# Performance work log

Hardware: AMD Instinct MI355X
Metric: run time of the kernel (lower is better)

Reference implementation:

```python
import jax, jax.numpy as jnp
import numpy as np

DIM = 64        # feature channels of x
HEADS = 4
POS_DIM = 3
NUM_IDS = 8
STR_IN = 512    # strength_linear input size
B, S, W = 4, 1024, 8   # batch, sequence (S1), source-views (S2)


def setup_inputs() -> dict:
    key = jax.random.key(0)
    ks = jax.random.split(key, 18)
    stdv = 1.0 / np.sqrt(DIM * DIM)  # embedding init per module
    d8 = DIM // 8
    u = lambda k, shp, s: jax.random.uniform(k, shp, jnp.float32, -s, s)
    return {
        "x": jax.random.normal(ks[0], (B, DIM, S, W), jnp.float32),
        "pos": jax.random.normal(ks[1], (B, S, POS_DIM), jnp.float32),
        "strength": jax.random.normal(ks[2], (STR_IN,), jnp.float32),
        "embed_id1": 3,
        "q_emb_w": u(ks[3], (NUM_IDS, DIM * DIM), stdv),
        "k_emb_w": u(ks[4], (NUM_IDS, DIM * DIM), stdv),
        "v_emb_w": u(ks[5], (NUM_IDS, DIM * DIM), stdv),
        "pos_w1": u(ks[6], (POS_DIM, POS_DIM), 1.0 / np.sqrt(POS_DIM)),
        "pos_b1": u(ks[7], (POS_DIM,), 1.0 / np.sqrt(POS_DIM)),
        "pos_w2": u(ks[8], (d8, POS_DIM), 1.0 / np.sqrt(POS_DIM)),
        "pos_b2": u(ks[9], (d8,), 1.0 / np.sqrt(POS_DIM)),
        "head_w": u(ks[10], (HEADS, d8), 1.0 / np.sqrt(d8)),
        "head_b": u(ks[11], (HEADS,), 1.0 / np.sqrt(d8)),
        "gate": jnp.ones((HEADS,), jnp.float32),
        "out_w": u(ks[12], (DIM, DIM), 1.0 / np.sqrt(DIM)),
        "out_b": u(ks[13], (DIM,), 1.0 / np.sqrt(DIM)),
        "str_w": u(ks[14], (DIM, STR_IN), 1.0 / np.sqrt(STR_IN)),
        "str_b": u(ks[15], (DIM,), 1.0 / np.sqrt(STR_IN)),
    }


def reference(x, pos, strength, embed_id1, q_emb_w, k_emb_w, v_emb_w,
              pos_w1, pos_b1, pos_w2, pos_b2, head_w, head_b, gate,
              out_w, out_b, str_w, str_b):
    # strength projection: Linear(512, dim)
    s = strength @ str_w.T + str_b                    # [dim]
    xt = jnp.transpose(x, (0, 2, 3, 1))               # [B, S, W, dim]
    qe = q_emb_w[embed_id1].reshape(DIM, DIM)
    ke = k_emb_w[embed_id1].reshape(DIM, DIM)
    ve = v_emb_w[embed_id1].reshape(DIM, DIM)

    def proj(emb):
        y = xt @ emb.T + s                            # [B, S, W, dim]
        # collapse (W, dim) -> (heads, head_dim), heads to axis 1
        y = y.reshape(B, S, HEADS, -1)
        return jnp.transpose(y, (0, 2, 1, 3))         # [B, H, S, hd]

    q, k, v = proj(qe), proj(ke), proj(ve)
    hd = q.shape[-1]
    attn = jax.nn.softmax(jnp.einsum("bhsd,bhtd->bhst", q, k) / np.sqrt(hd), axis=-1)

    # relative-position attention branch
    ph = jax.nn.relu(pos @ pos_w1.T + pos_b1) @ pos_w2.T + pos_b2   # [B, S, dim//8]
    diff = ph[:, :, None, :] - ph[:, None, :, :]                    # [B, S, S, dim//8]
    pos_attn = jnp.transpose(diff @ head_w.T + head_b, (0, 3, 1, 2))
    pos_attn = jax.nn.softmax(pos_attn, axis=-1)                    # [B, H, S, S]

    g = jax.nn.sigmoid(gate).reshape(1, -1, 1, 1)
    attn = (1.0 - g) * attn + g * pos_attn
    attn = attn / jnp.sum(attn, axis=-1, keepdims=True)

    out = jnp.einsum("bhst,bhtd->bhsd", attn, v)      # [B, H, S, hd]
    out = jnp.transpose(out, (0, 2, 1, 3)).reshape(B, S, W, DIM)
    return out @ out_w.T + out_b                      # [B, S, W, dim]
```

## Files before the change

kernel.cpp:

```cpp
#include <hip/hip_runtime.h>
#include <math.h>
#include <stdint.h>

#define B_ 4
#define S_ 1024
#define F_ 512
#define HD 128
#define SOFT_C 4.0f

typedef __attribute__((ext_vector_type(8))) short short8;
typedef __attribute__((ext_vector_type(4))) float f32x4;
typedef __attribute__((ext_vector_type(4))) unsigned int u32x4;
typedef __attribute__((ext_vector_type(2))) unsigned int u32x2;

__device__ __forceinline__ unsigned short f2bf(float f) {
    unsigned int u = __float_as_uint(f);
    u = (u + 0x7FFFu + ((u >> 16) & 1u)) >> 16;
    return (unsigned short)u;
}
__device__ __forceinline__ float bf2f(unsigned int s) {
    return __uint_as_float(s << 16);
}
__device__ __forceinline__ void pack_hilo(const float* v, u32x4& hi, u32x4& lo) {
    #pragma unroll
    for (int p = 0; p < 4; ++p) {
        unsigned int h0 = f2bf(v[2 * p]), h1 = f2bf(v[2 * p + 1]);
        float l0 = v[2 * p] - bf2f(h0), l1 = v[2 * p + 1] - bf2f(h1);
        hi[p] = h0 | (h1 << 16);
        lo[p] = (unsigned int)f2bf(l0) | ((unsigned int)f2bf(l1) << 16);
    }
}

__global__ __launch_bounds__(256) void k_prep(
    const int* __restrict__ embed_id,
    const float* __restrict__ qw, const float* __restrict__ kw,
    const float* __restrict__ vw, const float* __restrict__ ow,
    const float* __restrict__ pos,
    const float* __restrict__ pw1, const float* __restrict__ pb1,
    const float* __restrict__ pw2, const float* __restrict__ pb2,
    const float* __restrict__ head_w,
    const float* __restrict__ strength, const float* __restrict__ str_w,
    const float* __restrict__ str_b,
    unsigned short* __restrict__ packs,
    float* __restrict__ sv, float* __restrict__ svq,
    float* __restrict__ p_g)
{
    __shared__ float red_s[4][4];
    __shared__ float inv_s[4];
    const int blk = blockIdx.x, tid = threadIdx.x;
    const float SCALE = 0.08838834764831845f;

    if (blk < 4) {
        const int id = embed_id[0];
        const float* src = (blk == 0 ? qw + id * 4096 : blk == 1 ? kw + id * 4096
                            : blk == 2 ? vw + id * 4096 : ow);
        const float scale = (blk == 0) ? SCALE : 1.0f;
        unsigned short* hi = packs + blk * 8192;
        unsigned short* lo = hi + 4096;
        for (int i = tid; i < 4096; i += 256) {
            float v = src[i] * scale;
            unsigned short h = f2bf(v);
            hi[i] = h;
            lo[i] = f2bf(v - bf2f(h));
        }
    } else if (blk < 8) {
        const int b = blk - 4;
        const int wv = tid >> 6;
        float w1_[9], b1_[3], w2_[24], b2_[8], hw_[32];
        #pragma unroll
        for (int i = 0; i < 9; ++i)  w1_[i] = pw1[i];
        #pragma unroll
        for (int i = 0; i < 3; ++i)  b1_[i] = pb1[i];
        #pragma unroll
        for (int i = 0; i < 24; ++i) w2_[i] = pw2[i];
        #pragma unroll
        for (int i = 0; i < 8; ++i)  b2_[i] = pb2[i];
        #pragma unroll
        for (int i = 0; i < 32; ++i) hw_[i] = head_w[i];

        float ev[4][4];
        float ps[4] = {0.f, 0.f, 0.f, 0.f};
        #pragma unroll
        for (int k = 0; k < 4; ++k) {
            const int t = k * 256 + tid;
            float p0 = pos[(b * S_ + t) * 3 + 0];
            float p1 = pos[(b * S_ + t) * 3 + 1];
            float p2 = pos[(b * S_ + t) * 3 + 2];
            float h0 = fmaxf(0.f, p0 * w1_[0] + p1 * w1_[1] + p2 * w1_[2] + b1_[0]);
            float h1 = fmaxf(0.f, p0 * w1_[3] + p1 * w1_[4] + p2 * w1_[5] + b1_[1]);
            float h2 = fmaxf(0.f, p0 * w1_[6] + p1 * w1_[7] + p2 * w1_[8] + b1_[2]);
            float ph[8];
            #pragma unroll
            for (int o8 = 0; o8 < 8; ++o8)
                ph[o8] = h0 * w2_[o8 * 3] + h1 * w2_[o8 * 3 + 1] + h2 * w2_[o8 * 3 + 2] + b2_[o8];
            #pragma unroll
            for (int h = 0; h < 4; ++h) {
                float A = 0.f;
                #pragma unroll
                for (int o8 = 0; o8 < 8; ++o8) A += ph[o8] * hw_[h * 8 + o8];
                ev[k][h] = __expf(-A - 1.0f);
                ps[h] += ev[k][h];
            }
        }
        #pragma unroll
        for (int h = 0; h < 4; ++h)
            #pragma unroll
            for (int off = 1; off < 64; off <<= 1)
                ps[h] += __shfl_xor(ps[h], off);
        if ((tid & 63) == 0)
            #pragma unroll
            for (int h = 0; h < 4; ++h) red_s[wv][h] = ps[h];
        __syncthreads();
        if (tid < 4)
            inv_s[tid] = 1.f / (red_s[0][tid] + red_s[1][tid] + red_s[2][tid] + red_s[3][tid]);
        __syncthreads();
        #pragma unroll
        for (int k = 0; k < 4; ++k)
            #pragma unroll
            for (int h = 0; h < 4; ++h)
                p_g[(b * 4 + h) * S_ + k * 256 + tid] = ev[k][h] * inv_s[h];
    } else {
        __shared__ float part_s[4][64];
        const int c = tid & 63, pr = tid >> 6;
        const float* wrow = str_w + c * 512 + pr * 128;
        const float* st   = strength + pr * 128;
        float acc = 0.f;
        #pragma unroll
        for (int j4 = 0; j4 < 32; ++j4) {
            f32x4 wv4 = *(const f32x4*)(wrow + j4 * 4);
            f32x4 s4  = *(const f32x4*)(st + j4 * 4);
            acc += wv4[0] * s4[0] + wv4[1] * s4[1] + wv4[2] * s4[2] + wv4[3] * s4[3];
        }
        part_s[pr][c] = acc;
        __syncthreads();
        if (tid < 64) {
            float v = part_s[0][tid] + part_s[1][tid] + part_s[2][tid]
                    + part_s[3][tid] + str_b[tid];
            sv[tid] = v;
            svq[tid] = v * SCALE;
        }
    }
}

__global__ __launch_bounds__(256) void k_qkv(
    const float* __restrict__ x,
    const unsigned short* __restrict__ packs,
    const float* __restrict__ sv, const float* __restrict__ svq,
    const float* __restrict__ p_g,
    unsigned short* __restrict__ yqh, unsigned short* __restrict__ ykh,
    unsigned short* __restrict__ yvt2, float* __restrict__ xbar)
{
    __shared__ float xr_s[4][8];
    const int tid  = threadIdx.x;
    const int wv   = tid >> 6;
    const int lane = tid & 63;
    const int quad = lane >> 4;
    const int l15  = lane & 15;

    if (blockIdx.x >= 512) {
        const int bi = blockIdx.x - 512;
        const int b = bi >> 6, c = bi & 63;
        const float* xc = x + (size_t)b * 524288 + c * 8192;
        const float* pb = p_g + b * 4096;
        float acc[8] = {};
        #pragma unroll
        for (int rr = 0; rr < 4; ++rr) {
            const int s = tid * 4 + rr;
            f32x4 x0 = *(const f32x4*)(xc + s * 8);
            f32x4 x1 = *(const f32x4*)(xc + s * 8 + 4);
            float p0 = pb[s], p1 = pb[1024 + s], p2 = pb[2048 + s], p3 = pb[3072 + s];
            acc[0] += p0 * x0[0]; acc[1] += p0 * x0[1];
            acc[2] += p1 * x0[2]; acc[3] += p1 * x0[3];
            acc[4] += p2 * x1[0]; acc[5] += p2 * x1[1];
            acc[6] += p3 * x1[2]; acc[7] += p3 * x1[3];
        }
        #pragma unroll
        for (int j = 0; j < 8; ++j)
            #pragma unroll
            for (int off = 1; off < 64; off <<= 1)
                acc[j] += __shfl_xor(acc[j], off);
        if (lane == 0)
            #pragma unroll
            for (int j = 0; j < 8; ++j) xr_s[wv][j] = acc[j];
        __syncthreads();
        if (tid < 8)
            xbar[(b * 8 + tid) * 64 + c] = xr_s[0][tid] + xr_s[1][tid]
                                         + xr_s[2][tid] + xr_s[3][tid];
        return;
    }

    const int r0   = blockIdx.x * 64 + wv * 16;
    const int b    = r0 >> 13;
    const int rloc = (r0 & 8191) + l15;
    const float* xb = x + (size_t)b * 524288;

    u32x4 xhi[2], xlo[2];
    #pragma unroll
    for (int kc = 0; kc < 2; ++kc) {
        float xv[8];
        #pragma unroll
        for (int j = 0; j < 8; ++j)
            xv[j] = xb[(kc * 32 + quad * 8 + j) * 8192 + rloc];
        pack_hilo(xv, xhi[kc], xlo[kc]);
    }

    float svq_l[4], sv_l[4];
    #pragma unroll
    for (int nt = 0; nt < 4; ++nt) {
        svq_l[nt] = svq[nt * 16 + l15];
        sv_l[nt]  = sv[nt * 16 + l15];
    }
    f32x4 svA[4];
    #pragma unroll
    for (int mt = 0; mt < 4; ++mt)
        svA[mt] = *(const f32x4*)(sv + mt * 16 + quad * 4);

    int idxq[4];
    #pragma unroll
    for (int rr = 0; rr < 4; ++rr) {
        const int rl = quad * 4 + rr;
        const int w_ = rl & 7;
        const int s_loc = ((r0 & 8191) >> 3) + (rl >> 3);
        idxq[rr] = (b * 4 + (w_ >> 1)) * 131072 + s_loc * 128 + (w_ & 1) * 64 + l15;
    }
    const int row_g = r0 + l15;
    const int s_idx = (row_g >> 3) & 1023;
    const int w_idx = row_g & 7;
    const int bh    = b * 4 + (w_idx >> 1);
    const int dbase = (w_idx & 1) * 64;
    unsigned short* vtb = yvt2 + (size_t)bh * 131072 + (s_idx >> 6) * 8192
                        + (size_t)dbase * 64 + (s_idx & 63);

    #pragma unroll
    for (int mat = 0; mat < 2; ++mat) {
        const unsigned short* mh = packs + mat * 8192;
        const unsigned short* ml = mh + 4096;
        f32x4 acc[4] = {};
        #pragma unroll
        for (int kc = 0; kc < 2; ++kc)
            #pragma unroll
            for (int nt = 0; nt < 4; ++nt) {
                const int off = (nt * 16 + l15) * 64 + kc * 32 + quad * 8;
                u32x4 ehi = *(const u32x4*)(mh + off);
                u32x4 elo = *(const u32x4*)(ml + off);
                acc[nt] = __builtin_amdgcn_mfma_f32_16x16x32_bf16(
                    __builtin_bit_cast(short8, xhi[kc]),
                    __builtin_bit_cast(short8, ehi), acc[nt], 0, 0, 0);
                acc[nt] = __builtin_amdgcn_mfma_f32_16x16x32_bf16(
                    __builtin_bit_cast(short8, xlo[kc]),
                    __builtin_bit_cast(short8, ehi), acc[nt], 0, 0, 0);
                acc[nt] = __builtin_amdgcn_mfma_f32_16x16x32_bf16(
                    __builtin_bit_cast(short8, xhi[kc]),
                    __builtin_bit_cast(short8, elo), acc[nt], 0, 0, 0);
            }
        unsigned short* y = (mat == 0 ? yqh : ykh);
        const float* svp = (mat == 0 ? svq_l : sv_l);
        #pragma unroll
        for (int nt = 0; nt < 4; ++nt)
            #pragma unroll
            for (int rr = 0; rr < 4; ++rr)
                y[(size_t)idxq[rr] + nt * 16] = f2bf(acc[nt][rr] + svp[nt]);
    }
    {
        const unsigned short* mh = packs + 2 * 8192;
        const unsigned short* ml = mh + 4096;
        f32x4 acc[4] = {};
        #pragma unroll
        for (int kc = 0; kc < 2; ++kc)
            #pragma unroll
            for (int mt = 0; mt < 4; ++mt) {
                const int off = (mt * 16 + l15) * 64 + kc * 32 + quad * 8;
                u32x4 ehi = *(const u32x4*)(mh + off);
                u32x4 elo = *(const u32x4*)(ml + off);
                acc[mt] = __builtin_amdgcn_mfma_f32_16x16x32_bf16(
                    __builtin_bit_cast(short8, ehi),
                    __builtin_bit_cast(short8, xhi[kc]), acc[mt], 0, 0, 0);
                acc[mt] = __builtin_amdgcn_mfma_f32_16x16x32_bf16(
                    __builtin_bit_cast(short8, ehi),
                    __builtin_bit_cast(short8, xlo[kc]), acc[mt], 0, 0, 0);
                acc[mt] = __builtin_amdgcn_mfma_f32_16x16x32_bf16(
                    __builtin_bit_cast(short8, elo),
                    __builtin_bit_cast(short8, xhi[kc]), acc[mt], 0, 0, 0);
            }
        #pragma unroll
        for (int mt = 0; mt < 4; ++mt)
            #pragma unroll
            for (int rr = 0; rr < 4; ++rr) {
                const int c = mt * 16 + quad * 4 + rr;
                vtb[(size_t)c * 64] = f2bf(acc[mt][rr] + svA[mt][rr]);
            }
    }
}

__global__ __launch_bounds__(256, 4) void k_attn(
    const unsigned short* __restrict__ yqh, const unsigned short* __restrict__ ykh,
    const unsigned short* __restrict__ yvt2,
    const float* __restrict__ xbar, const float* __restrict__ vw,
    const int* __restrict__ embed_id, const float* __restrict__ sv_g,
    const float* __restrict__ gate,
    const unsigned short* __restrict__ packs,
    const float* __restrict__ ow, const float* __restrict__ ob,
    float* __restrict__ out)
{
    __shared__ __align__(16) unsigned short kx[64 * 136];
    __shared__ __align__(16) unsigned short vx[128 * 72];
    __shared__ float vbar_s[128];
    __shared__ float vproj_s[128];
    __shared__ float lsh[2][16];

    const int tid  = threadIdx.x;
    const int w    = tid >> 6;
    const int lane = tid & 63;
    const int quad = lane >> 4;
    const int l15  = lane & 15;
    const int bh = blockIdx.x & 15, qt = blockIdx.x >> 4;
    const int b = bh >> 2, h = bh & 3;
    const int s0 = qt * 16;
    const int th = w >> 1;
    const int dh = w & 1;

    const unsigned short* ykb = ykh + (size_t)bh * 131072;
    const unsigned short* yvb = yvt2 + (size_t)bh * 131072;
    const float gf = 1.f / (1.f + __expf(-gate[h]));

    if (tid < 128) {
        const int c = tid & 63, wloc = tid >> 6;
        const float* ver = vw + embed_id[0] * 4096 + c * 64;
        const float* xbr = xbar + (b * 8 + h * 2 + wloc) * 64;
        float a = sv_g[c];
        #pragma unroll
        for (int j4 = 0; j4 < 16; ++j4) {
            f32x4 e4 = *(const f32x4*)(ver + j4 * 4);
            f32x4 x4 = *(const f32x4*)(xbr + j4 * 4);
            a += e4[0] * x4[0] + e4[1] * x4[1] + e4[2] * x4[2] + e4[3] * x4[3];
        }
        vbar_s[wloc * 64 + c] = a;
    }

    u32x4 qf[4];
    #pragma unroll
    for (int kc = 0; kc < 4; ++kc)
        qf[kc] = *(const u32x4*)(yqh + (size_t)bh * 131072
                 + (s0 + l15) * 128 + kc * 32 + quad * 8);

    u32x4 kst[4], vst[4];
    #pragma unroll
    for (int r = 0; r < 4; ++r) {
        kst[r] = *(const u32x4*)(ykb + r * 2048 + tid * 8);
        vst[r] = *(const u32x4*)(yvb + r * 2048 + tid * 8);
    }

    __syncthreads();
    if (tid < 128) {
        const int cp = tid & 63, w2 = tid >> 6;
        const float* owr = ow + cp * 64;
        const float* vb = vbar_s + w2 * 64;
        float a = 0.f;
        #pragma unroll
        for (int j4 = 0; j4 < 16; ++j4) {
            f32x4 o4 = *(const f32x4*)(owr + j4 * 4);
            f32x4 v4 = *(const f32x4*)(vb + j4 * 4);
            a += o4[0] * v4[0] + o4[1] * v4[1] + o4[2] * v4[2] + o4[3] * v4[3];
        }
        vproj_s[tid] = gf * a + ob[cp];
    }

    f32x4 o[4] = {};
    float lsum = 0.f;
    const int srcA = ((quad & 1) << 5) + l15;
    const int t0loc = th * 32;

    for (int it = 0; it < 16; ++it) {
        #pragma unroll
        for (int r = 0; r < 4; ++r) {
            const int off = r * 2048 + tid * 8;
            *(u32x4*)&kx[(off >> 7) * 136 + (off & 127)] = kst[r];
            *(u32x4*)&vx[(off >> 6) * 72 + (off & 63)] = vst[r];
        }
        __syncthreads();
        if (it < 15) {
            const unsigned short* ksrc = ykb + (it + 1) * 8192;
            const unsigned short* vsrc = yvb + (it + 1) * 8192;
            #pragma unroll
            for (int r = 0; r < 4; ++r)
                kst[r] = *(const u32x4*)(ksrc + r * 2048 + tid * 8);
            #pragma unroll
            for (int r = 0; r < 4; ++r)
                vst[r] = *(const u32x4*)(vsrc + r * 2048 + tid * 8);
        }

        f32x4 sa0 = {}, sa1 = {};
        #pragma unroll
        for (int kc = 0; kc < 4; ++kc) {
            u32x4 a0 = *(const u32x4*)&kx[(t0loc + l15) * 136 + kc * 32 + quad * 8];
            sa0 = __builtin_amdgcn_mfma_f32_16x16x32_bf16(
                __builtin_bit_cast(short8, a0),
                __builtin_bit_cast(short8, qf[kc]), sa0, 0, 0, 0);
        }
        #pragma unroll
        for (int kc = 0; kc < 4; ++kc) {
            u32x4 a1 = *(const u32x4*)&kx[(t0loc + 16 + l15) * 136 + kc * 32 + quad * 8];
            sa1 = __builtin_amdgcn_mfma_f32_16x16x32_bf16(
                __builtin_bit_cast(short8, a1),
                __builtin_bit_cast(short8, qf[kc]), sa1, 0, 0, 0);
        }

        float p0[4], p1[4];
        #pragma unroll
        for (int r = 0; r < 4; ++r) {
            p0[r] = __expf(sa0[r] - SOFT_C);
            p1[r] = __expf(sa1[r] - SOFT_C);
            lsum += p0[r] + p1[r];
        }

        unsigned int pk00 = (unsigned int)f2bf(p0[0]) | ((unsigned int)f2bf(p0[1]) << 16);
        unsigned int pk01 = (unsigned int)f2bf(p0[2]) | ((unsigned int)f2bf(p0[3]) << 16);
        unsigned int pk10 = (unsigned int)f2bf(p1[0]) | ((unsigned int)f2bf(p1[1]) << 16);
        unsigned int pk11 = (unsigned int)f2bf(p1[2]) | ((unsigned int)f2bf(p1[3]) << 16);
        unsigned int sel0 = (quad < 2) ? pk00 : pk10;
        unsigned int sel1 = (quad < 2) ? pk01 : pk11;
        u32x4 pf;
        pf[0] = (unsigned int)__shfl((int)sel0, srcA);
        pf[1] = (unsigned int)__shfl((int)sel1, srcA);
        pf[2] = (unsigned int)__shfl((int)sel0, srcA + 16);
        pf[3] = (unsigned int)__shfl((int)sel1, srcA + 16);

        #pragma unroll
        for (int dt = 0; dt < 4; ++dt) {
            u32x4 vf = *(const u32x4*)&vx[(dh * 64 + dt * 16 + l15) * 72
                                           + t0loc + quad * 8];
            o[dt] = __builtin_amdgcn_mfma_f32_16x16x32_bf16(
                __builtin_bit_cast(short8, vf),
                __builtin_bit_cast(short8, pf), o[dt], 0, 0, 0);
        }
        __syncthreads();
    }

    lsum += __shfl_xor(lsum, 16);
    lsum += __shfl_xor(lsum, 32);
    float* cmb = (float*)kx;
    if (th == 1) {
        #pragma unroll
        for (int dt = 0; dt < 4; ++dt)
            *(f32x4*)&cmb[(dh * 16 + l15) * 68 + dt * 16 + quad * 4] = o[dt];
        if (quad == 0) lsh[dh][l15] = lsum;
    }
    __syncthreads();
    if (th == 0) {
        #pragma unroll
        for (int dt = 0; dt < 4; ++dt) {
            f32x4 p = *(const f32x4*)&cmb[(dh * 16 + l15) * 68 + dt * 16 + quad * 4];
            o[dt] += p;
        }
        lsum += lsh[dh][l15];
        const float cf = (1.f - gf) / lsum;

        unsigned short* yst = (unsigned short*)vx + dh * 4352;
        #pragma unroll
        for (int dt = 0; dt < 4; ++dt) {
            unsigned int hh[4];
            unsigned short ll[4];
            #pragma unroll
            for (int r = 0; r < 4; ++r) {
                float y = cf * o[dt][r];
                hh[r] = f2bf(y);
                ll[r] = f2bf(y - bf2f(hh[r]));
            }
            const int dloc = dt * 16 + quad * 4;
            u32x2 ph_, pl_;
            ph_[0] = hh[0] | (hh[1] << 16);
            ph_[1] = hh[2] | (hh[3] << 16);
            pl_[0] = (unsigned int)ll[0] | ((unsigned int)ll[1] << 16);
            pl_[1] = (unsigned int)ll[2] | ((unsigned int)ll[3] << 16);
            *(u32x2*)&yst[l15 * 68 + dloc] = ph_;
            *(u32x2*)&yst[1088 + l15 * 68 + dloc] = pl_;
        }
        u32x4 ybh[2], ybl[2];
        #pragma unroll
        for (int kc = 0; kc < 2; ++kc) {
            ybh[kc] = *(const u32x4*)&yst[l15 * 68 + kc * 32 + quad * 8];
            ybl[kc] = *(const u32x4*)&yst[1088 + l15 * 68 + kc * 32 + quad * 8];
        }
        const unsigned short* owh = packs + 3 * 8192;
        const unsigned short* owl = owh + 4096;
        f32x4 accp[4] = {};
        #pragma unroll
        for (int kc = 0; kc < 2; ++kc)
            #pragma unroll
            for (int mt = 0; mt < 4; ++mt) {
                const int off = (mt * 16 + l15) * 64 + kc * 32 + quad * 8;
                u32x4 ahi = *(const u32x4*)(owh + off);
                u32x4 alo = *(const u32x4*)(owl + off);
                accp[mt] = __builtin_amdgcn_mfma_f32_16x16x32_bf16(
                    __builtin_bit_cast(short8, ahi),
                    __builtin_bit_cast(short8, ybh[kc]), accp[mt], 0, 0, 0);
                accp[mt] = __builtin_amdgcn_mfma_f32_16x16x32_bf16(
                    __builtin_bit_cast(short8, ahi),
                    __builtin_bit_cast(short8, ybl[kc]), accp[mt], 0, 0, 0);
                accp[mt] = __builtin_amdgcn_mfma_f32_16x16x32_bf16(
                    __builtin_bit_cast(short8, alo),
                    __builtin_bit_cast(short8, ybh[kc]), accp[mt], 0, 0, 0);
            }
        const int sQ = s0 + l15;
        float* op = out + ((size_t)((b * S_ + sQ) * 8 + 2 * h + dh)) * 64;
        #pragma unroll
        for (int mt = 0; mt < 4; ++mt) {
            f32x4 vp = *(const f32x4*)&vproj_s[dh * 64 + mt * 16 + quad * 4];
            f32x4 rv = accp[mt] + vp;
            *(f32x4*)(op + mt * 16 + quad * 4) = rv;
        }
    }
}

extern "C" void kernel_launch(void* const* d_in, const int* in_sizes, int n_in,
                              void* d_out, int out_size, void* d_ws, size_t ws_size,
                              hipStream_t stream) {
    (void)in_sizes; (void)n_in; (void)out_size; (void)ws_size;
    const float* x        = (const float*)d_in[0];
    const float* pos      = (const float*)d_in[1];
    const float* strength = (const float*)d_in[2];
    const int*   embed_id = (const int*)d_in[3];
    const float* qw       = (const float*)d_in[4];
    const float* kw       = (const float*)d_in[5];
    const float* vw       = (const float*)d_in[6];
    const float* pw1      = (const float*)d_in[7];
    const float* pb1      = (const float*)d_in[8];
    const float* pw2      = (const float*)d_in[9];
    const float* pb2      = (const float*)d_in[10];
    const float* head_w   = (const float*)d_in[11];
    const float* gate     = (const float*)d_in[13];
    const float* out_w    = (const float*)d_in[14];
    const float* out_b    = (const float*)d_in[15];
    const float* str_w    = (const float*)d_in[16];
    const float* str_b    = (const float*)d_in[17];
    float* out = (float*)d_out;

    unsigned short* yqh   = (unsigned short*)d_ws;
    unsigned short* ykh   = yqh + 2097152;
    unsigned short* yvt2  = ykh + 2097152;
    unsigned short* packs = yvt2 + 2097152;
    float* sv   = (float*)(packs + 8 * 4096);
    float* svq  = sv + 64;
    float* p_g  = svq + 64;
    float* xbar = p_g + 16384;

    k_prep<<<9, 256, 0, stream>>>(embed_id, qw, kw, vw, out_w, pos,
                                  pw1, pb1, pw2, pb2, head_w,
                                  strength, str_w, str_b, packs, sv, svq, p_g);
    k_qkv<<<768, 256, 0, stream>>>(x, packs, sv, svq, p_g, yqh, ykh, yvt2, xbar);
    k_attn<<<1024, 256, 0, stream>>>(yqh, ykh, yvt2, xbar, vw, embed_id, sv,
                                     gate, packs, out_w, out_b, out);
}
```

Baseline: 165.5 us.

## Store K/V in MFMA fragment order and stream them from global without LDS

The QKV kernel now writes K and V directly in the per-lane MFMA fragment layout, so the attention kernel can load operands straight from global memory into registers with a one-step register prefetch instead of staging tiles through LDS with barriers. Each attention block now handles 32 queries (each wave owns a 16-query x 64-dim slice over all keys), so the cross-wave partial-sum combine and the grid halves to 512 blocks. This removes LDS traffic and per-iteration syncthreads, but each wave now reads K/V from global/L2 on its own, raising cache traffic and register pressure. The occupancy hint in launch bounds is also dropped.

```diff
diff --git a/kernel.cpp b/kernel.cpp
--- a/kernel.cpp
+++ b/kernel.cpp
@@ -147,8 +147,8 @@
     const unsigned short* __restrict__ packs,
     const float* __restrict__ sv, const float* __restrict__ svq,
     const float* __restrict__ p_g,
-    unsigned short* __restrict__ yqh, unsigned short* __restrict__ ykh,
-    unsigned short* __restrict__ yvt2, float* __restrict__ xbar)
+    unsigned short* __restrict__ yqh, unsigned short* __restrict__ kfrag,
+    unsigned short* __restrict__ vfrag, float* __restrict__ xbar)
 {
     __shared__ float xr_s[4][8];
     const int tid  = threadIdx.x;
@@ -216,20 +216,25 @@
         svA[mt] = *(const f32x4*)(sv + mt * 16 + quad * 4);
 
     int idxq[4];
+    size_t idxk[4];
     #pragma unroll
     for (int rr = 0; rr < 4; ++rr) {
         const int rl = quad * 4 + rr;
-        const int w_ = rl & 7;
-        const int s_loc = ((r0 & 8191) >> 3) + (rl >> 3);
-        idxq[rr] = (b * 4 + (w_ >> 1)) * 131072 + s_loc * 128 + (w_ & 1) * 64 + l15;
+        const int row_g2 = r0 + rl;
+        const int s = (row_g2 & 8191) >> 3;
+        const int w_ = row_g2 & 7;
+        const int bh = ((row_g2 >> 13) * 4) + (w_ >> 1);
+        idxq[rr] = (bh * 131072) + s * 128 + (w_ & 1) * 64 + l15;
+        idxk[rr] = (size_t)(bh * 64 + (s >> 4)) * 2048 + (s & 15) * 8
+                 + (w_ & 1) * 1024 + (l15 >> 3) * 128 + (l15 & 7);
     }
     const int row_g = r0 + l15;
     const int s_idx = (row_g >> 3) & 1023;
     const int w_idx = row_g & 7;
-    const int bh    = b * 4 + (w_idx >> 1);
+    const int bhv   = (row_g >> 13) * 4 + (w_idx >> 1);
     const int dbase = (w_idx & 1) * 64;
-    unsigned short* vtb = yvt2 + (size_t)bh * 131072 + (s_idx >> 6) * 8192
-                        + (size_t)dbase * 64 + (s_idx & 63);
+    const size_t vbase = (size_t)(bhv * 32 + (s_idx >> 5)) * 4096
+                       + ((s_idx >> 3) & 3) * 8 + (s_idx & 7);
 
     #pragma unroll
     for (int mat = 0; mat < 2; ++mat) {
@@ -253,13 +258,19 @@
                     __builtin_bit_cast(short8, xhi[kc]),
                     __builtin_bit_cast(short8, elo), acc[nt], 0, 0, 0);
             }
-        unsigned short* y = (mat == 0 ? yqh : ykh);
-        const float* svp = (mat == 0 ? svq_l : sv_l);
-        #pragma unroll
-        for (int nt = 0; nt < 4; ++nt)
-            #pragma unroll
-            for (int rr = 0; rr < 4; ++rr)
-                y[(size_t)idxq[rr] + nt * 16] = f2bf(acc[nt][rr] + svp[nt]);
+        if (mat == 0) {
+            #pragma unroll
+            for (int nt = 0; nt < 4; ++nt)
+                #pragma unroll
+                for (int rr = 0; rr < 4; ++rr)
+                    yqh[(size_t)idxq[rr] + nt * 16] = f2bf(acc[nt][rr] + svq_l[nt]);
+        } else {
+            #pragma unroll
+            for (int nt = 0; nt < 4; ++nt)
+                #pragma unroll
+                for (int rr = 0; rr < 4; ++rr)
+                    kfrag[idxk[rr] + nt * 256] = f2bf(acc[nt][rr] + sv_l[nt]);
+        }
     }
     {
         const unsigned short* mh = packs + 2 * 8192;
@@ -286,15 +297,16 @@
         for (int mt = 0; mt < 4; ++mt)
             #pragma unroll
             for (int rr = 0; rr < 4; ++rr) {
-                const int c = mt * 16 + quad * 4 + rr;
-                vtb[(size_t)c * 64] = f2bf(acc[mt][rr] + svA[mt][rr]);
+                const int dd = dbase + mt * 16 + quad * 4 + rr;
+                vfrag[vbase + (dd >> 4) * 512 + (dd & 15) * 32] =
+                    f2bf(acc[mt][rr] + svA[mt][rr]);
             }
     }
 }
 
-__global__ __launch_bounds__(256, 4) void k_attn(
-    const unsigned short* __restrict__ yqh, const unsigned short* __restrict__ ykh,
-    const unsigned short* __restrict__ yvt2,
+__global__ __launch_bounds__(256) void k_attn(
+    const unsigned short* __restrict__ yqh, const unsigned short* __restrict__ kfrag,
+    const unsigned short* __restrict__ vfrag,
     const float* __restrict__ xbar, const float* __restrict__ vw,
     const int* __restrict__ embed_id, const float* __restrict__ sv_g,
     const float* __restrict__ gate,
@@ -302,11 +314,9 @@
     const float* __restrict__ ow, const float* __restrict__ ob,
     float* __restrict__ out)
 {
-    __shared__ __align__(16) unsigned short kx[64 * 136];
-    __shared__ __align__(16) unsigned short vx[128 * 72];
+    __shared__ __align__(16) unsigned short yst_s[4 * 4352];
     __shared__ float vbar_s[128];
     __shared__ float vproj_s[128];
-    __shared__ float lsh[2][16];
 
     const int tid  = threadIdx.x;
     const int w    = tid >> 6;
@@ -315,12 +325,12 @@
     const int l15  = lane & 15;
     const int bh = blockIdx.x & 15, qt = blockIdx.x >> 4;
     const int b = bh >> 2, h = bh & 3;
-    const int s0 = qt * 16;
-    const int th = w >> 1;
+    const int s0 = qt * 32;
+    const int qh = w >> 1;
     const int dh = w & 1;
 
-    const unsigned short* ykb = ykh + (size_t)bh * 131072;
-    const unsigned short* yvb = yvt2 + (size_t)bh * 131072;
+    const unsigned short* kb = kfrag + (size_t)bh * 131072;
+    const unsigned short* vb = vfrag + (size_t)bh * 131072;
     const float gf = 1.f / (1.f + __expf(-gate[h]));
 
     if (tid < 128) {
@@ -336,74 +346,72 @@
         }
         vbar_s[wloc * 64 + c] = a;
     }
-
-    u32x4 qf[4];
-    #pragma unroll
-    for (int kc = 0; kc < 4; ++kc)
-        qf[kc] = *(const u32x4*)(yqh + (size_t)bh * 131072
-                 + (s0 + l15) * 128 + kc * 32 + quad * 8);
-
-    u32x4 kst[4], vst[4];
-    #pragma unroll
-    for (int r = 0; r < 4; ++r) {
-        kst[r] = *(const u32x4*)(ykb + r * 2048 + tid * 8);
-        vst[r] = *(const u32x4*)(yvb + r * 2048 + tid * 8);
-    }
-
     __syncthreads();
     if (tid < 128) {
         const int cp = tid & 63, w2 = tid >> 6;
         const float* owr = ow + cp * 64;
-        const float* vb = vbar_s + w2 * 64;
+        const float* vbp = vbar_s + w2 * 64;
         float a = 0.f;
         #pragma unroll
         for (int j4 = 0; j4 < 16; ++j4) {
             f32x4 o4 = *(const f32x4*)(owr + j4 * 4);
-            f32x4 v4 = *(const f32x4*)(vb + j4 * 4);
+            f32x4 v4 = *(const f32x4*)(vbp + j4 * 4);
             a += o4[0] * v4[0] + o4[1] * v4[1] + o4[2] * v4[2] + o4[3] * v4[3];
         }
         vproj_s[tid] = gf * a + ob[cp];
     }
+    __syncthreads();
+
+    u32x4 qf[4];
+    #pragma unroll
+    for (int kc = 0; kc < 4; ++kc)
+        qf[kc] = *(const u32x4*)(yqh + (size_t)bh * 131072
+                 + (s0 + qh * 16 + l15) * 128 + kc * 32 + quad * 8);
+
+    const int kl = quad * 128 + l15 * 8;
+    const int vl = l15 * 32 + quad * 8;
 
     f32x4 o[4] = {};
     float lsum = 0.f;
     const int srcA = ((quad & 1) << 5) + l15;
-    const int t0loc = th * 32;
-
-    for (int it = 0; it < 16; ++it) {
-        #pragma unroll
-        for (int r = 0; r < 4; ++r) {
-            const int off = r * 2048 + tid * 8;
-            *(u32x4*)&kx[(off >> 7) * 136 + (off & 127)] = kst[r];
-            *(u32x4*)&vx[(off >> 6) * 72 + (off & 63)] = vst[r];
-        }
-        __syncthreads();
-        if (it < 15) {
-            const unsigned short* ksrc = ykb + (it + 1) * 8192;
-            const unsigned short* vsrc = yvb + (it + 1) * 8192;
-            #pragma unroll
-            for (int r = 0; r < 4; ++r)
-                kst[r] = *(const u32x4*)(ksrc + r * 2048 + tid * 8);
-            #pragma unroll
-            for (int r = 0; r < 4; ++r)
-                vst[r] = *(const u32x4*)(vsrc + r * 2048 + tid * 8);
+
+    u32x4 k0c[4], k1c[4], vvc[4];
+    #pragma unroll
+    for (int kc = 0; kc < 4; ++kc) {
+        k0c[kc] = *(const u32x4*)(kb + kc * 512 + kl);
+        k1c[kc] = *(const u32x4*)(kb + 2048 + kc * 512 + kl);
+    }
+    #pragma unroll
+    for (int dt = 0; dt < 4; ++dt)
+        vvc[dt] = *(const u32x4*)(vb + (dh * 4 + dt) * 512 + vl);
+
+    #pragma unroll 2
+    for (int it = 0; it < 32; ++it) {
+        u32x4 k0n[4], k1n[4], vvn[4];
+        if (it < 31) {
+            const unsigned short* kbn = kb + (size_t)(it + 1) * 4096;
+            const unsigned short* vbn = vb + (size_t)(it + 1) * 4096;
+            #pragma unroll
+            for (int kc = 0; kc < 4; ++kc) {
+                k0n[kc] = *(const u32x4*)(kbn + kc * 512 + kl);
+                k1n[kc] = *(const u32x4*)(kbn + 2048 + kc * 512 + kl);
+            }
+            #pragma unroll
+            for (int dt = 0; dt < 4; ++dt)
+                vvn[dt] = *(const u32x4*)(vbn + (dh * 4 + dt) * 512 + vl);
         }
 
         f32x4 sa0 = {}, sa1 = {};
         #pragma unroll
-        for (int kc = 0; kc < 4; ++kc) {
-            u32x4 a0 = *(const u32x4*)&kx[(t0loc + l15) * 136 + kc * 32 + quad * 8];
+        for (int kc = 0; kc < 4; ++kc)
             sa0 = __builtin_amdgcn_mfma_f32_16x16x32_bf16(
-                __builtin_bit_cast(short8, a0),
+                __builtin_bit_cast(short8, k0c[kc]),
                 __builtin_bit_cast(short8, qf[kc]), sa0, 0, 0, 0);
-        }
-        #pragma unroll
-        for (int kc = 0; kc < 4; ++kc) {
-            u32x4 a1 = *(const u32x4*)&kx[(t0loc + 16 + l15) * 136 + kc * 32 + quad * 8];
+        #pragma unroll
+        for (int kc = 0; kc < 4; ++kc)
             sa1 = __builtin_amdgcn_mfma_f32_16x16x32_bf16(
-                __builtin_bit_cast(short8, a1),
+                __builtin_bit_cast(short8, k1c[kc]),
                 __builtin_bit_cast(short8, qf[kc]), sa1, 0, 0, 0);
-        }
 
         float p0[4], p1[4];
         #pragma unroll
@@ -426,89 +434,74 @@
         pf[3] = (unsigned int)__shfl((int)sel1, srcA + 16);
 
         #pragma unroll
-        for (int dt = 0; dt < 4; ++dt) {
-            u32x4 vf = *(const u32x4*)&vx[(dh * 64 + dt * 16 + l15) * 72
-                                           + t0loc + quad * 8];
+        for (int dt = 0; dt < 4; ++dt)
             o[dt] = __builtin_amdgcn_mfma_f32_16x16x32_bf16(
-                __builtin_bit_cast(short8, vf),
+                __builtin_bit_cast(short8, vvc[dt]),
                 __builtin_bit_cast(short8, pf), o[dt], 0, 0, 0);
-        }
-        __syncthreads();
+
+        #pragma unroll
+        for (int kc = 0; kc < 4; ++kc) { k0c[kc] = k0n[kc]; k1c[kc] = k1n[kc]; }
+        #pragma unroll
+        for (int dt = 0; dt < 4; ++dt) vvc[dt] = vvn[dt];
     }
 
     lsum += __shfl_xor(lsum, 16);
     lsum += __shfl_xor(lsum, 32);
-    float* cmb = (float*)kx;
-    if (th == 1) {
-        #pragma unroll
-        for (int dt = 0; dt < 4; ++dt)
-            *(f32x4*)&cmb[(dh * 16 + l15) * 68 + dt * 16 + quad * 4] = o[dt];
-        if (quad == 0) lsh[dh][l15] = lsum;
-    }
-    __syncthreads();
-    if (th == 0) {
-        #pragma unroll
-        for (int dt = 0; dt < 4; ++dt) {
-            f32x4 p = *(const f32x4*)&cmb[(dh * 16 + l15) * 68 + dt * 16 + quad * 4];
-            o[dt] += p;
-        }
-        lsum += lsh[dh][l15];
-        const float cf = (1.f - gf) / lsum;
-
-        unsigned short* yst = (unsigned short*)vx + dh * 4352;
-        #pragma unroll
-        for (int dt = 0; dt < 4; ++dt) {
-            unsigned int hh[4];
-            unsigned short ll[4];
-            #pragma unroll
-            for (int r = 0; r < 4; ++r) {
-                float y = cf * o[dt][r];
-                hh[r] = f2bf(y);
-                ll[r] = f2bf(y - bf2f(hh[r]));
-            }
-            const int dloc = dt * 16 + quad * 4;
-            u32x2 ph_, pl_;
-            ph_[0] = hh[0] | (hh[1] << 16);
-            ph_[1] = hh[2] | (hh[3] << 16);
-            pl_[0] = (unsigned int)ll[0] | ((unsigned int)ll[1] << 16);
-            pl_[1] = (unsigned int)ll[2] | ((unsigned int)ll[3] << 16);
-            *(u32x2*)&yst[l15 * 68 + dloc] = ph_;
-            *(u32x2*)&yst[1088 + l15 * 68 + dloc] = pl_;
-        }
-        u32x4 ybh[2], ybl[2];
-        #pragma unroll
-        for (int kc = 0; kc < 2; ++kc) {
-            ybh[kc] = *(const u32x4*)&yst[l15 * 68 + kc * 32 + quad * 8];
-            ybl[kc] = *(const u32x4*)&yst[1088 + l15 * 68 + kc * 32 + quad * 8];
-        }
-        const unsigned short* owh = packs + 3 * 8192;
-        const unsigned short* owl = owh + 4096;
-        f32x4 accp[4] = {};
-        #pragma unroll
-        for (int kc = 0; kc < 2; ++kc)
-            #pragma unroll
-            for (int mt = 0; mt < 4; ++mt) {
-                const int off = (mt * 16 + l15) * 64 + kc * 32 + quad * 8;
-                u32x4 ahi = *(const u32x4*)(owh + off);
-                u32x4 alo = *(const u32x4*)(owl + off);
-                accp[mt] = __builtin_amdgcn_mfma_f32_16x16x32_bf16(
-                    __builtin_bit_cast(short8, ahi),
-                    __builtin_bit_cast(short8, ybh[kc]), accp[mt], 0, 0, 0);
-                accp[mt] = __builtin_amdgcn_mfma_f32_16x16x32_bf16(
-                    __builtin_bit_cast(short8, ahi),
-                    __builtin_bit_cast(short8, ybl[kc]), accp[mt], 0, 0, 0);
-                accp[mt] = __builtin_amdgcn_mfma_f32_16x16x32_bf16(
-                    __builtin_bit_cast(short8, alo),
-                    __builtin_bit_cast(short8, ybh[kc]), accp[mt], 0, 0, 0);
-            }
-        const int sQ = s0 + l15;
-        float* op = out + ((size_t)((b * S_ + sQ) * 8 + 2 * h + dh)) * 64;
+    const float cf = (1.f - gf) / lsum;
+
+    unsigned short* yst = yst_s + w * 4352;
+    #pragma unroll
+    for (int dt = 0; dt < 4; ++dt) {
+        unsigned int hh[4];
+        unsigned short ll[4];
+        #pragma unroll
+        for (int r = 0; r < 4; ++r) {
+            float y = cf * o[dt][r];
+            hh[r] = f2bf(y);
+            ll[r] = f2bf(y - bf2f(hh[r]));
+        }
+        const int dloc = dt * 16 + quad * 4;
+        u32x2 ph_, pl_;
+        ph_[0] = hh[0] | (hh[1] << 16);
+        ph_[1] = hh[2] | (hh[3] << 16);
+        pl_[0] = (unsigned int)ll[0] | ((unsigned int)ll[1] << 16);
+        pl_[1] = (unsigned int)ll[2] | ((unsigned int)ll[3] << 16);
+        *(u32x2*)&yst[l15 * 68 + dloc] = ph_;
+        *(u32x2*)&yst[1088 + l15 * 68 + dloc] = pl_;
+    }
+    u32x4 ybh[2], ybl[2];
+    #pragma unroll
+    for (int kc = 0; kc < 2; ++kc) {
+        ybh[kc] = *(const u32x4*)&yst[l15 * 68 + kc * 32 + quad * 8];
+        ybl[kc] = *(const u32x4*)&yst[1088 + l15 * 68 + kc * 32 + quad * 8];
+    }
+    const unsigned short* owh = packs + 3 * 8192;
+    const unsigned short* owl = owh + 4096;
+    f32x4 accp[4] = {};
+    #pragma unroll
+    for (int kc = 0; kc < 2; ++kc)
         #pragma unroll
         for (int mt = 0; mt < 4; ++mt) {
-            f32x4 vp = *(const f32x4*)&vproj_s[dh * 64 + mt * 16 + quad * 4];
-            f32x4 rv = accp[mt] + vp;
-            *(f32x4*)(op + mt * 16 + quad * 4) = rv;
-        }
+            const int off = (mt * 16 + l15) * 64 + kc * 32 + quad * 8;
+            u32x4 ahi = *(const u32x4*)(owh + off);
+            u32x4 alo = *(const u32x4*)(owl + off);
+            accp[mt] = __builtin_amdgcn_mfma_f32_16x16x32_bf16(
+                __builtin_bit_cast(short8, ahi),
+                __builtin_bit_cast(short8, ybh[kc]), accp[mt], 0, 0, 0);
+            accp[mt] = __builtin_amdgcn_mfma_f32_16x16x32_bf16(
+                __builtin_bit_cast(short8, ahi),
+                __builtin_bit_cast(short8, ybl[kc]), accp[mt], 0, 0, 0);
+            accp[mt] = __builtin_amdgcn_mfma_f32_16x16x32_bf16(
+                __builtin_bit_cast(short8, alo),
+                __builtin_bit_cast(short8, ybh[kc]), accp[mt], 0, 0, 0);
+        }
+    const int sQ = s0 + qh * 16 + l15;
+    float* op = out + ((size_t)((b * S_ + sQ) * 8 + 2 * h + dh)) * 64;
+    #pragma unroll
+    for (int mt = 0; mt < 4; ++mt) {
+        f32x4 vp = *(const f32x4*)&vproj_s[dh * 64 + mt * 16 + quad * 4];
+        f32x4 rv = accp[mt] + vp;
+        *(f32x4*)(op + mt * 16 + quad * 4) = rv;
     }
 }
 
@@ -536,9 +529,9 @@
     float* out = (float*)d_out;
 
     unsigned short* yqh   = (unsigned short*)d_ws;
-    unsigned short* ykh   = yqh + 2097152;
-    unsigned short* yvt2  = ykh + 2097152;
-    unsigned short* packs = yvt2 + 2097152;
+    unsigned short* kfrag = yqh + 2097152;
+    unsigned short* vfrag = kfrag + 2097152;
+    unsigned short* packs = vfrag + 2097152;
     float* sv   = (float*)(packs + 8 * 4096);
     float* svq  = sv + 64;
     float* p_g  = svq + 64;
@@ -547,7 +540,7 @@
     k_prep<<<9, 256, 0, stream>>>(embed_id, qw, kw, vw, out_w, pos,
                                   pw1, pb1, pw2, pb2, head_w,
                                   strength, str_w, str_b, packs, sv, svq, p_g);
-    k_qkv<<<768, 256, 0, stream>>>(x, packs, sv, svq, p_g, yqh, ykh, yvt2, xbar);
-    k_attn<<<1024, 256, 0, stream>>>(yqh, ykh, yvt2, xbar, vw, embed_id, sv,
-                                     gate, packs, out_w, out_b, out);
-}
+    k_qkv<<<768, 256, 0, stream>>>(x, packs, sv, svq, p_g, yqh, kfrag, vfrag, xbar);
+    k_attn<<<512, 256, 0, stream>>>(yqh, kfrag, vfrag, xbar, vw, embed_id, sv,
+                                    gate, packs, out_w, out_b, out);
+}
```

New measurement: 160.4 us. -3.1%, faster.
